# Optimization experiments

Measured on AMD Instinct MI355X. Metric: run time of the kernel, lower is better.

Reference implementation:

```python
import jax, jax.numpy as jnp
import numpy as np

N, E, DIN, HID, G, L = 50000, 200000, 128, 128, 64, 6
H1, H2 = 8, 4
EPS_LN, EPS_BN = 1e-5, 1e-5


def setup_inputs() -> dict:
    key = jax.random.key(0)
    ks = iter(jax.random.split(key, 32))
    def nrm(shape, scale=0.05):
        return jax.random.normal(next(ks), shape, dtype=jnp.float32) * scale
    z = lambda *s: jnp.zeros(s, jnp.float32)
    o = lambda *s: jnp.ones(s, jnp.float32)
    return {
        'x': jax.random.normal(next(ks), (N, DIN), dtype=jnp.float32),
        'edge_index': jax.random.randint(next(ks), (2, E), 0, N),
        'batch': jnp.sort(jax.random.randint(next(ks), (N,), 0, G)),
        'W1': nrm((DIN, H1 * HID)), 'a_src1': nrm((H1, HID)), 'a_dst1': nrm((H1, HID)), 'b1': z(H1 * HID),
        'W2': nrm((H1 * HID, H2 * HID)), 'a_src2': nrm((H2, HID)), 'a_dst2': nrm((H2, HID)), 'b2': z(H2 * HID),
        'W3': nrm((H2 * HID, HID)), 'b3': z(HID),
        'wq': nrm((L, HID, HID)), 'bq': z(L, HID), 'wk': nrm((L, HID, HID)), 'bk': z(L, HID),
        'wv': nrm((L, HID, HID)), 'bv': z(L, HID), 'wo': nrm((L, HID, HID)), 'bo': z(L, HID),
        'ln1g': o(L, HID), 'ln1b': z(L, HID), 'ln2g': o(L, HID), 'ln2b': z(L, HID),
        'wf1': nrm((L, HID, 4 * HID)), 'bf1': z(L, 4 * HID), 'wf2': nrm((L, 4 * HID, HID)), 'bf2': z(L, HID),
        'bn1_g': o(2 * HID), 'bn1_b': z(2 * HID),
        'fc1_w': nrm((2 * HID, HID // 2)), 'fc1_b': z(HID // 2),
        'bn2_g': o(HID // 2), 'bn2_b': z(HID // 2),
        'fc2_w': nrm((HID // 2, 2)), 'fc2_b': z(2),
    }


def _ln(x, g, b):
    mu = x.mean(-1, keepdims=True)
    v = ((x - mu) ** 2).mean(-1, keepdims=True)
    return (x - mu) * jax.lax.rsqrt(v + EPS_LN) * g + b


def _gat(x, src, dst, W, a_s, a_d, b, heads):
    # PyG GATConv: message src -> dst, segment softmax over incoming edges per dst.
    h = (x @ W).reshape(x.shape[0], heads, -1)           # [N, H, C]
    e = jax.nn.leaky_relu((h * a_s).sum(-1)[src] + (h * a_d).sum(-1)[dst], 0.2)  # [E, H]
    m = jax.ops.segment_max(e, dst, num_segments=N)
    ex = jnp.exp(e - jnp.where(jnp.isfinite(m), m, 0.0)[dst])
    s = jax.ops.segment_sum(ex, dst, num_segments=N)
    alpha = ex / (s[dst] + 1e-16)
    out = jax.ops.segment_sum(alpha[:, :, None] * h[src], dst, num_segments=N)
    return out.reshape(N, -1) + b


def _forward(x, edge_index, batch, W1, a_src1, a_dst1, b1, W2, a_src2, a_dst2, b2, W3, b3,
             wq, bq, wk, bk, wv, bv, wo, bo, ln1g, ln1b, ln2g, ln2b, wf1, bf1, wf2, bf2,
             bn1_g, bn1_b, fc1_w, fc1_b, bn2_g, bn2_b, fc2_w, fc2_b):
    loop = jnp.arange(N, dtype=edge_index.dtype)
    src = jnp.concatenate([edge_index[0], loop])          # add self-loops (PyG default)
    dst = jnp.concatenate([edge_index[1], loop])
    h = jax.nn.elu(_gat(x, src, dst, W1, a_src1, a_dst1, b1, H1))
    h = jax.nn.elu(_gat(h, src, dst, W2, a_src2, a_dst2, b2, H2))
    # GCNConv with symmetric normalization (self-loops already included)
    deg = jax.ops.segment_sum(jnp.ones(src.shape, h.dtype), dst, num_segments=N)
    dinv = jnp.where(deg > 0, jax.lax.rsqrt(jnp.maximum(deg, 1e-12)), 0.0)
    norm = dinv[src] * dinv[dst]
    h = jax.nn.elu(jax.ops.segment_sum(norm[:, None] * (h @ W3)[src], dst, num_segments=N) + b3)
    # TransformerEncoder over seq_len=1 (h3.unsqueeze(1)): softmax over one key == 1,
    # so MHA output == Wo @ (Wv h + bv) + bo exactly; q/k have no effect on the output.
    for l in range(L):
        sa = (h @ wv[l] + bv[l]) @ wo[l] + bo[l]
        h = _ln(h + sa, ln1g[l], ln1b[l])
        ff = jax.nn.gelu(h @ wf1[l] + bf1[l], approximate=False) @ wf2[l] + bf2[l]
        h = _ln(h + ff, ln2g[l], ln2b[l])
    # global mean / max pool over graphs
    cnt = jax.ops.segment_sum(jnp.ones((N,), h.dtype), batch, num_segments=G)
    hm = jax.ops.segment_sum(h, batch, num_segments=G) / jnp.maximum(cnt, 1.0)[:, None]
    hx = jax.ops.segment_max(h, batch, num_segments=G)
    hx = jnp.where(jnp.isfinite(hx), hx, 0.0)
    hc = jnp.concatenate([hm, hx], axis=1)                # [G, 2*HID]
    bn_s = 1.0 / np.sqrt(1.0 + EPS_BN)                    # eval BN: running stats (0, 1)
    hc = hc * bn_s * bn1_g + bn1_b
    hc = jax.nn.elu(hc @ fc1_w + fc1_b)
    hc = hc * bn_s * bn2_g + bn2_b
    return hc @ fc2_w + fc2_b                             # [G, 2]


def reference(x, edge_index, batch, W1, a_src1, a_dst1, b1, W2, a_src2, a_dst2, b2, W3, b3,
              wq, bq, wk, bk, wv, bv, wo, bo, ln1g, ln1b, ln2g, ln2b, wf1, bf1, wf2, bf2,
              bn1_g, bn1_b, fc1_w, fc1_b, bn2_g, bn2_b, fc2_w, fc2_b):
    return _forward(x, edge_index, batch, W1, a_src1, a_dst1, b1, W2, a_src2, a_dst2, b2, W3, b3,
                    wq, bq, wk, bk, wv, bv, wo, bo, ln1g, ln1b, ln2g, ln2b, wf1, bf1, wf2, bf2,
                    bn1_g, bn1_b, fc1_w, fc1_b, bn2_g, bn2_b, fc2_w, fc2_b)
```

## Files before the change

### kernel.cpp

```cpp
#include <hip/hip_runtime.h>
#include <hip/hip_bf16.h>
#include <math.h>

#define NN 50000
#define EE 200000
#define ET 250000
#define GG 64
#define LL 6

using short8 = __attribute__((ext_vector_type(8))) short;
using f32x4  = __attribute__((ext_vector_type(4))) float;
typedef unsigned short ushortT;

__device__ __forceinline__ float elu1(float x) { return x > 0.f ? x : expm1f(x); }
__device__ __forceinline__ float gelu_exact(float x) {
    return 0.5f * x * (1.f + erff(x * 0.70710678118654752440f));
}
__device__ __forceinline__ short f2bf(float f) {
    __hip_bfloat16 h = __float2bfloat16(f);
    return *reinterpret_cast<short*>(&h);
}
__device__ __forceinline__ float bf2f(ushortT u) {
    return __uint_as_float(((unsigned)u) << 16);
}

__global__ void count_deg_kernel(const int* __restrict__ ei, int* __restrict__ deg) {
    int e = blockIdx.x * 256 + threadIdx.x;
    if (e >= ET) return;
    int dst = (e < EE) ? ei[EE + e] : (e - EE);
    atomicAdd(&deg[dst], 1);
}

__global__ void scan_kernel(const int* __restrict__ deg, int* __restrict__ row_ptr, int n) {
    __shared__ int s[1024];
    int tid = threadIdx.x;
    const int per = (n + 1023) / 1024;
    int lo = tid * per, hi = min(lo + per, n);
    int sum = 0;
    for (int i = lo; i < hi; i++) sum += deg[i];
    s[tid] = sum;
    __syncthreads();
    for (int off = 1; off < 1024; off <<= 1) {
        int t = (tid >= off) ? s[tid - off] : 0;
        __syncthreads();
        s[tid] += t;
        __syncthreads();
    }
    int run = s[tid] - sum;
    for (int i = lo; i < hi; i++) { row_ptr[i] = run; run += deg[i]; }
    if (tid == 1023) row_ptr[n] = s[1023];
}

__global__ void fill_csr_kernel(const int* __restrict__ ei, const int* __restrict__ row_ptr,
                                int* __restrict__ cursor, int* __restrict__ edge_src) {
    int e = blockIdx.x * 256 + threadIdx.x;
    if (e >= ET) return;
    int src, dst;
    if (e < EE) { src = ei[e]; dst = ei[EE + e]; }
    else        { src = e - EE; dst = e - EE; }
    int pos = atomicAdd(&cursor[dst], 1);
    edge_src[row_ptr[dst] + pos] = src;
}

__global__ void dinv_kernel(const int* __restrict__ row_ptr, float* __restrict__ dinv) {
    int n = blockIdx.x * 256 + threadIdx.x;
    if (n >= NN) return;
    int d = row_ptr[n + 1] - row_ptr[n];
    dinv[n] = (d > 0) ? rsqrtf((float)d) : 0.f;
}

__global__ void wvwo_kernel(const float* __restrict__ wv, const float* __restrict__ wo,
                            const float* __restrict__ bv, const float* __restrict__ bo,
                            float* __restrict__ Wvo, float* __restrict__ bvo) {
    int l = blockIdx.y;
    const float* Wv = wv + l * 16384;
    const float* Wo = wo + l * 16384;
    int tid = blockIdx.x * 256 + threadIdx.x;
    if (tid < 16384) {
        int r = tid >> 7, c = tid & 127;
        float s = 0.f;
        for (int k = 0; k < 128; k++) s += Wv[r * 128 + k] * Wo[k * 128 + c];
        Wvo[l * 16384 + tid] = s;
    }
    if (blockIdx.x == 0 && threadIdx.x < 128) {
        int c = threadIdx.x;
        float s = bo[l * 128 + c];
        for (int k = 0; k < 128; k++) s += bv[l * 128 + k] * Wo[k * 128 + c];
        bvo[l * 128 + c] = s;
    }
}

__global__ void bprep_kernel(const float* __restrict__ B, short* __restrict__ Bp,
                             int K, int N, int ldb, long srcStride) {
    int layer = blockIdx.y;
    const float* Bsrc = B + srcStride * layer;
    short* Bd = Bp + (size_t)K * N * layer;
    int total = (K >> 5) * (N >> 4) * 64;
    int tid = blockIdx.x * 256 + threadIdx.x;
    if (tid >= total) return;
    int l = tid & 63;
    int rest = tid >> 6;
    int kbc = K >> 5;
    int kb = rest % kbc;
    int c16 = rest / kbc;
    int n = c16 * 16 + (l & 15);
    int kbase = kb * 32 + (l >> 4) * 8;
    short v[8];
#pragma unroll
    for (int j = 0; j < 8; j++) v[j] = f2bf(Bsrc[(size_t)(kbase + j) * ldb + n]);
    *(uint4*)(Bd + (size_t)tid * 8) = *(uint4*)v;
}

__global__ void cast_bf16_kernel(const float* __restrict__ in, short* __restrict__ out, int n4) {
    int i = blockIdx.x * 256 + threadIdx.x;
    if (i >= n4) return;
    float4 v = *(const float4*)(in + (size_t)i * 4);
    short s[4] = { f2bf(v.x), f2bf(v.y), f2bf(v.z), f2bf(v.w) };
    *(uint2*)(out + (size_t)i * 4) = *(uint2*)s;
}

template <int EPI, bool BIAS, bool OUTBF16, int NSPLIT, int KBC>
__global__ __launch_bounds__(256) void gemm_bf16_kernel(
    const short* __restrict__ A, const short* __restrict__ Bp,
    const float* __restrict__ bias, void* __restrict__ Cv,
    const float* __restrict__ a_s, const float* __restrict__ a_d,
    float* __restrict__ as_out, float* __restrict__ ad_out, int asH,
    const ushortT* __restrict__ Rres, const float* __restrict__ lng,
    const float* __restrict__ lnb, float* __restrict__ Qout,
    __hip_bfloat16* __restrict__ Qbout,
    int M, int K, int Nc) {
    __shared__ short Bs[(KBC > 0) ? KBC * 4096 : 8192];
    int t = threadIdx.x;
    int w = t >> 6, l = t & 63;
    int ln = l & 15, lq = l >> 4;
    int MBceil = (M + 63) >> 6;
    int bx = blockIdx.x;
    int xcd = bx & 7, idx = bx >> 3;
    int t2 = idx % NSPLIT;
    int mb = (idx / NSPLIT) * 8 + xcd;
    if (mb >= MBceil) return;
    int bm = mb * 64 + w * 16;
    int arow = bm + ln;
    bool aok = arow < M;
    int rowb = bm + lq * 4;
    const short* Ap = A + (size_t)arow * K + lq * 8;

    f32x4 acc[8];
#pragma unroll
    for (int j = 0; j < 8; j++) acc[j] = (f32x4){0.f, 0.f, 0.f, 0.f};

    if constexpr (KBC > 0) {
        {
            const uint4* src = (const uint4*)(Bp + (size_t)t2 * KBC * 4096);
            uint4* dst = (uint4*)Bs;
#pragma unroll
            for (int i = 0; i < KBC * 2; i++)
                dst[i * 256 + t] = src[i * 256 + t];
        }
        short8 af[KBC];
#pragma unroll
        for (int kb = 0; kb < KBC; kb++)
            af[kb] = aok ? *(const short8*)(Ap + kb * 32) : (short8){0,0,0,0,0,0,0,0};
        __syncthreads();
#pragma unroll
        for (int kb = 0; kb < KBC; kb++)
#pragma unroll
            for (int ct = 0; ct < 8; ct++) {
                short8 bfr = *(const short8*)(Bs + ((ct * KBC + kb) * 64 + l) * 8);
                acc[ct] = __builtin_amdgcn_mfma_f32_16x16x32_bf16(af[kb], bfr, acc[ct], 0, 0, 0);
            }
    } else {
        int kbc = K >> 5;
        int sct = t >> 5, spart = t & 31;
        auto stage = [&](int buf, int kb) {
            const uint4* src = (const uint4*)(Bp + ((size_t)(t2 * 8 + sct) * kbc + kb) * 512);
            uint4* dst = (uint4*)(Bs + buf * 4096 + sct * 512);
            dst[spart * 2]     = src[spart * 2];
            dst[spart * 2 + 1] = src[spart * 2 + 1];
        };
        stage(0, 0);
        __syncthreads();
        for (int kb = 0; kb < kbc; kb++) {
            if (kb + 1 < kbc) stage((kb + 1) & 1, kb + 1);
            short8 af = aok ? *(const short8*)(Ap + kb * 32) : (short8){0,0,0,0,0,0,0,0};
            const short* bsb = Bs + (kb & 1) * 4096;
#pragma unroll
            for (int ct = 0; ct < 8; ct++) {
                short8 bfr = *(const short8*)(bsb + (ct * 64 + l) * 8);
                acc[ct] = __builtin_amdgcn_mfma_f32_16x16x32_bf16(af, bfr, acc[ct], 0, 0, 0);
            }
            __syncthreads();
        }
    }

    if (EPI == 2) {
        const float* asv = a_s + t2 * 128;
        const float* adv = a_d + t2 * 128;
#pragma unroll
        for (int reg = 0; reg < 4; reg++) {
            float vs = 0.f, vd = 0.f;
#pragma unroll
            for (int ct = 0; ct < 8; ct++) {
                int colL = ct * 16 + ln;
                float av = acc[ct][reg];
                vs += av * asv[colL];
                vd += av * adv[colL];
            }
            vs += __shfl_xor(vs, 1); vs += __shfl_xor(vs, 2);
            vs += __shfl_xor(vs, 4); vs += __shfl_xor(vs, 8);
            vd += __shfl_xor(vd, 1); vd += __shfl_xor(vd, 2);
            vd += __shfl_xor(vd, 4); vd += __shfl_xor(vd, 8);
            int row = rowb + reg;
            if (ln == 0 && row < M) {
                as_out[(size_t)row * asH + t2] = vs;
                ad_out[(size_t)row * asH + t2] = vd;
            }
        }
    }
    if (EPI == 3) {
        float v[8][4];
#pragma unroll
        for (int ct = 0; ct < 8; ct++) {
            int col = ct * 16 + ln;
            float bv_ = bias[col];
#pragma unroll
            for (int reg = 0; reg < 4; reg++) {
                int row = rowb + reg;
                float r = (row < M) ? bf2f(Rres[(size_t)row * 128 + col]) : 0.f;
                v[ct][reg] = acc[ct][reg] + bv_ + r;
            }
        }
#pragma unroll
        for (int reg = 0; reg < 4; reg++) {
            float s = 0.f;
#pragma unroll
            for (int ct = 0; ct < 8; ct++) s += v[ct][reg];
            s += __shfl_xor(s, 1); s += __shfl_xor(s, 2);
            s += __shfl_xor(s, 4); s += __shfl_xor(s, 8);
            float mean = s * (1.f / 128.f);
            float s2 = 0.f;
#pragma unroll
            for (int ct = 0; ct < 8; ct++) { float d = v[ct][reg] - mean; s2 += d * d; }
            s2 += __shfl_xor(s2, 1); s2 += __shfl_xor(s2, 2);
            s2 += __shfl_xor(s2, 4); s2 += __shfl_xor(s2, 8);
            float rstd = rsqrtf(s2 * (1.f / 128.f) + 1e-5f);
            int row = rowb + reg;
            if (row < M) {
#pragma unroll
                for (int ct = 0; ct < 8; ct++) {
                    int col = ct * 16 + ln;
                    float o = (v[ct][reg] - mean) * rstd * lng[col] + lnb[col];
                    Qbout[(size_t)row * 128 + col] = __float2bfloat16(o);
                    if (Qout) Qout[(size_t)row * 128 + col] = o;
                }
            }
        }
    }
    if (EPI == 0 || EPI == 1 || EPI == 2) {
#pragma unroll
        for (int ct = 0; ct < 8; ct++) {
            int col = t2 * 128 + ct * 16 + ln;
            float bv_ = BIAS ? bias[col] : 0.f;
#pragma unroll
            for (int reg = 0; reg < 4; reg++) {
                int row = rowb + reg;
                if (row < M) {
                    float v = acc[ct][reg] + bv_;
                    if (EPI == 1) v = gelu_exact(v);
                    if (OUTBF16)
                        ((__hip_bfloat16*)Cv)[(size_t)row * Nc + col] = __float2bfloat16(v);
                    else
                        ((float*)Cv)[(size_t)row * Nc + col] = v;
                }
            }
        }
    }
}

template <int H>
__global__ __launch_bounds__(256) void gat_alpha_kernel(
    const float* __restrict__ as_, const float* __restrict__ ad_,
    const int* __restrict__ row_ptr, const int* __restrict__ edge_src,
    float* __restrict__ exA, float* __restrict__ exS, int n_nodes) {
    const int GS = 64 / H;
    int node = blockIdx.x * 4 + (threadIdx.x >> 6);
    if (node >= n_nodes) return;
    int l = threadIdx.x & 63;
    int h = l / GS;
    int lig = l % GS;
    int start = row_ptr[node];
    int deg = row_ptr[node + 1] - start;
    float adn = ad_[(size_t)node * H + h];
    float m = -1e30f;
    for (int j = lig; j < deg; j += GS) {
        int s = edge_src[start + j];
        float e = as_[(size_t)s * H + h] + adn;
        e = e > 0.f ? e : 0.2f * e;
        m = fmaxf(m, e);
    }
#pragma unroll
    for (int mask = 1; mask < GS; mask <<= 1)
        m = fmaxf(m, __shfl_xor(m, mask));
    float S = 0.f;
    for (int j = lig; j < deg; j += GS) {
        int s = edge_src[start + j];
        float e = as_[(size_t)s * H + h] + adn;
        e = e > 0.f ? e : 0.2f * e;
        float ex = expf(e - m);
        exA[(size_t)(start + j) * H + h] = ex;
        S += ex;
    }
#pragma unroll
    for (int mask = 1; mask < GS; mask <<= 1)
        S += __shfl_xor(S, mask);
    if (lig == 0) exS[(size_t)node * H + h] = S;
}

template <int H>
__global__ __launch_bounds__(256) void gat_agg2_kernel(
    const ushortT* __restrict__ hpre, const float* __restrict__ exA,
    const float* __restrict__ exS, const float* __restrict__ bias,
    const int* __restrict__ row_ptr, const int* __restrict__ edge_src,
    __hip_bfloat16* __restrict__ out, int n_nodes) {
    const int CPT = H;
    int node = blockIdx.x * 2 + (threadIdx.x >> 7);
    if (node >= n_nodes) return;
    int tt = threadIdx.x & 127;
    int c0 = tt * CPT;
    int hb = c0 >> 7;
    int start = row_ptr[node];
    int deg = row_ptr[node + 1] - start;
    float acc[CPT];
#pragma unroll
    for (int c = 0; c < CPT; c++) acc[c] = 0.f;
    for (int j = 0; j < deg; j++) {
        int s = edge_src[start + j];
        float a = exA[(size_t)(start + j) * H + hb];
        const ushortT* hp = hpre + (size_t)s * (H * 128) + c0;
        float hv[CPT];
        if (CPT == 8) {
            uint4 u = *(const uint4*)hp;
            hv[0] = bf2f((ushortT)(u.x & 0xffff)); hv[1] = bf2f((ushortT)(u.x >> 16));
            hv[2] = bf2f((ushortT)(u.y & 0xffff)); hv[3] = bf2f((ushortT)(u.y >> 16));
            hv[4] = bf2f((ushortT)(u.z & 0xffff)); hv[5] = bf2f((ushortT)(u.z >> 16));
            hv[6] = bf2f((ushortT)(u.w & 0xffff)); hv[7] = bf2f((ushortT)(u.w >> 16));
        } else {
            uint2 u = *(const uint2*)hp;
            hv[0] = bf2f((ushortT)(u.x & 0xffff)); hv[1] = bf2f((ushortT)(u.x >> 16));
            hv[2] = bf2f((ushortT)(u.y & 0xffff)); hv[3] = bf2f((ushortT)(u.y >> 16));
        }
#pragma unroll
        for (int c = 0; c < CPT; c++) acc[c] += a * hv[c];
    }
    float inv = 1.f / (exS[(size_t)node * H + hb] + 1e-16f);
#pragma unroll
    for (int c = 0; c < CPT; c++)
        out[(size_t)node * (H * 128) + c0 + c] =
            __float2bfloat16(elu1(acc[c] * inv + bias[c0 + c]));
}

__global__ __launch_bounds__(256) void gcn_agg_kernel(
    const ushortT* __restrict__ hp, const float* __restrict__ dinv,
    const float* __restrict__ b3, const int* __restrict__ row_ptr,
    const int* __restrict__ edge_src,
    __hip_bfloat16* __restrict__ outb, int n_nodes) {
    int node = blockIdx.x * 2 + (threadIdx.x >> 7);
    int c = threadIdx.x & 127;
    if (node >= n_nodes) return;
    int start = row_ptr[node];
    int deg = row_ptr[node + 1] - start;
    float dn = dinv[node];
    float acc = 0.f;
    for (int j = 0; j < deg; j++) {
        int s = edge_src[start + j];
        acc += dinv[s] * dn * bf2f(hp[(size_t)s * 128 + c]);
    }
    outb[(size_t)node * 128 + c] = __float2bfloat16(elu1(acc + b3[c]));
}

__global__ void pool1_kernel(const float* __restrict__ Q, const int* __restrict__ batch,
                             float* __restrict__ psum, float* __restrict__ pmax, int n_nodes) {
    int g = blockIdx.x, seg = blockIdx.y;
    int c = threadIdx.x;
    int lo, hi;
    {
        int l = 0, h = n_nodes;
        while (l < h) { int mid = (l + h) >> 1; if (batch[mid] < g) l = mid + 1; else h = mid; }
        lo = l;
        l = lo; h = n_nodes;
        while (l < h) { int mid = (l + h) >> 1; if (batch[mid] < g + 1) l = mid + 1; else h = mid; }
        hi = l;
    }
    int len = hi - lo;
    int a = lo + (int)((long)len * seg / 8);
    int b = lo + (int)((long)len * (seg + 1) / 8);
    float s = 0.f, mx = -INFINITY;
    for (int n = a; n < b; n++) {
        float v = Q[(size_t)n * 128 + c];
        s += v;
        mx = fmaxf(mx, v);
    }
    psum[(g * 8 + seg) * 128 + c] = s;
    pmax[(g * 8 + seg) * 128 + c] = mx;
}

__global__ void pool2_kernel(const float* __restrict__ psum, const float* __restrict__ pmax,
                             const int* __restrict__ batch,
                             const float* __restrict__ bn1g, const float* __restrict__ bn1b,
                             float* __restrict__ hc, int n_nodes) {
    int g = blockIdx.x;
    int c = threadIdx.x;
    int lo, hi;
    {
        int l = 0, h = n_nodes;
        while (l < h) { int mid = (l + h) >> 1; if (batch[mid] < g) l = mid + 1; else h = mid; }
        lo = l;
        l = lo; h = n_nodes;
        while (l < h) { int mid = (l + h) >> 1; if (batch[mid] < g + 1) l = mid + 1; else h = mid; }
        hi = l;
    }
    int cnt = hi - lo;
    float s = 0.f, mx = -INFINITY;
    for (int seg = 0; seg < 8; seg++) {
        s += psum[(g * 8 + seg) * 128 + c];
        mx = fmaxf(mx, pmax[(g * 8 + seg) * 128 + c]);
    }
    float hm = s / fmaxf((float)cnt, 1.f);
    float hx = (cnt > 0 && isfinite(mx)) ? mx : 0.f;
    const float bn_s = 0.99999500003749968f;
    hc[g * 256 + c]       = hm * bn_s * bn1g[c] + bn1b[c];
    hc[g * 256 + 128 + c] = hx * bn_s * bn1g[128 + c] + bn1b[128 + c];
}

__global__ void head_kernel(const float* __restrict__ hc,
                            const float* __restrict__ fc1w, const float* __restrict__ fc1b,
                            const float* __restrict__ bn2g, const float* __restrict__ bn2b,
                            const float* __restrict__ fc2w, const float* __restrict__ fc2b,
                            float* __restrict__ out) {
    int g = blockIdx.x;
    int j = threadIdx.x;
    const float bn_s = 0.99999500003749968f;
    float acc = fc1b[j];
    for (int i = 0; i < 256; i++) acc += hc[g * 256 + i] * fc1w[i * 64 + j];
    acc = elu1(acc);
    acc = acc * bn_s * bn2g[j] + bn2b[j];
    __shared__ float sv[64];
    sv[j] = acc;
    __syncthreads();
    if (j < 2) {
        float o = fc2b[j];
        for (int i = 0; i < 64; i++) o += sv[i] * fc2w[i * 2 + j];
        out[g * 2 + j] = o;
    }
}

extern "C" void kernel_launch(void* const* d_in, const int* in_sizes, int n_in,
                              void* d_out, int out_size, void* d_ws, size_t ws_size,
                              hipStream_t stream) {
    const float* x    = (const float*)d_in[0];
    const int*   ei   = (const int*)d_in[1];
    const int*   batch= (const int*)d_in[2];
    const float* W1   = (const float*)d_in[3];
    const float* as1  = (const float*)d_in[4];
    const float* ad1  = (const float*)d_in[5];
    const float* b1   = (const float*)d_in[6];
    const float* W2   = (const float*)d_in[7];
    const float* as2  = (const float*)d_in[8];
    const float* ad2  = (const float*)d_in[9];
    const float* b2   = (const float*)d_in[10];
    const float* W3   = (const float*)d_in[11];
    const float* b3   = (const float*)d_in[12];
    const float* wv   = (const float*)d_in[17];
    const float* bv   = (const float*)d_in[18];
    const float* wo   = (const float*)d_in[19];
    const float* bo   = (const float*)d_in[20];
    const float* ln1g = (const float*)d_in[21];
    const float* ln1b = (const float*)d_in[22];
    const float* ln2g = (const float*)d_in[23];
    const float* ln2b = (const float*)d_in[24];
    const float* wf1  = (const float*)d_in[25];
    const float* bf1  = (const float*)d_in[26];
    const float* wf2  = (const float*)d_in[27];
    const float* bf2  = (const float*)d_in[28];
    const float* bn1g = (const float*)d_in[29];
    const float* bn1b = (const float*)d_in[30];
    const float* fc1w = (const float*)d_in[31];
    const float* fc1b = (const float*)d_in[32];
    const float* bn2g = (const float*)d_in[33];
    const float* bn2b = (const float*)d_in[34];
    const float* fc2w = (const float*)d_in[35];
    const float* fc2b = (const float*)d_in[36];
    float* out = (float*)d_out;

    char* wsb = (char*)d_ws;
    short* xb    = (short*)wsb;
    float* exAf  = (float*)wsb;
    float* exSf  = (float*)(wsb + 8000000);
    short* h1pre = (short*)(wsb + 12800000);
    short* h2pre = (short*)(wsb + 12800000);
    short* h3pre = (short*)(wsb + 12800000);
    short* FFb   = (short*)(wsb + 25600000);
    short* bh1   = (short*)(wsb + 115200000);
    short* bh2   = (short*)(wsb + 115200000);
    float* fQ    = (float*)(wsb + 128000000);
    short* Qb    = (short*)(wsb + 153600000);
    char* tail = wsb + 217600000;
    short* W1p  = (short*)tail;  tail += 262144;
    short* W2p  = (short*)tail;  tail += 1048576;
    short* W3p  = (short*)tail;  tail += 131072;
    short* Wvop = (short*)tail;  tail += 196608;
    short* wf1p = (short*)tail;  tail += 786432;
    short* wf2p = (short*)tail;  tail += 786432;
    float* Wvo  = (float*)tail;  tail += 393216;
    float* bvo  = (float*)tail;  tail += 3072;
    float* fAS  = (float*)tail;  tail += 1600000;
    float* fAD  = (float*)tail;  tail += 1600000;
    float* fDv  = (float*)tail;  tail += 200000;
    float* psum = (float*)tail;  tail += 262144;
    float* pmax = (float*)tail;  tail += 262144;
    float* fHC  = (float*)tail;  tail += 65536;
    int* iDeg   = (int*)tail;    tail += 200000;
    int* iRP    = (int*)tail;    tail += 200004;
    int* iCur   = (int*)tail;    tail += 200000;
    int* iES    = (int*)tail;    tail += 1000000;

    hipMemsetAsync(iDeg, 0, NN * sizeof(int), stream);
    hipMemsetAsync(iCur, 0, NN * sizeof(int), stream);

    count_deg_kernel<<<(ET + 255) / 256, 256, 0, stream>>>(ei, iDeg);
    scan_kernel<<<1, 1024, 0, stream>>>(iDeg, iRP, NN);
    fill_csr_kernel<<<(ET + 255) / 256, 256, 0, stream>>>(ei, iRP, iCur, iES);
    dinv_kernel<<<(NN + 255) / 256, 256, 0, stream>>>(iRP, fDv);

    wvwo_kernel<<<dim3(64, 6), 256, 0, stream>>>(wv, wo, bv, bo, Wvo, bvo);
    auto bprep = [&](const float* B, short* Bp, int K, int N, int ldb, long sStride, int layers) {
        int total = (K >> 5) * (N >> 4) * 64;
        dim3 grid((total + 255) / 256, layers);
        bprep_kernel<<<grid, 256, 0, stream>>>(B, Bp, K, N, ldb, sStride);
    };
    bprep(W1, W1p, 128, 1024, 1024, 0, 1);
    bprep(W2, W2p, 1024, 512, 512, 0, 1);
    bprep(W3, W3p, 512, 128, 128, 0, 1);
    bprep(Wvo, Wvop, 128, 128, 128, 16384, 6);
    bprep(wf1, wf1p, 128, 512, 512, 65536, 6);
    bprep(wf2, wf2p, 512, 128, 128, 65536, 6);
    cast_bf16_kernel<<<(NN * 128 / 4 + 255) / 256, 256, 0, stream>>>(x, xb, NN * 128 / 4);

    const int MB64 = (NN + 63) / 64;
    const int MBp = ((MB64 + 7) / 8) * 8;

    gemm_bf16_kernel<2, false, true, 8, 4><<<MBp * 8, 256, 0, stream>>>(
        xb, W1p, nullptr, h1pre, as1, ad1, fAS, fAD, 8,
        nullptr, nullptr, nullptr, nullptr, nullptr, NN, 128, 1024);
    gat_alpha_kernel<8><<<(NN + 3) / 4, 256, 0, stream>>>(
        fAS, fAD, iRP, iES, exAf, exSf, NN);
    gat_agg2_kernel<8><<<(NN + 1) / 2, 256, 0, stream>>>(
        (const ushortT*)h1pre, exAf, exSf, b1, iRP, iES, (__hip_bfloat16*)bh1, NN);
    gemm_bf16_kernel<2, false, true, 4, 0><<<MBp * 4, 256, 0, stream>>>(
        bh1, W2p, nullptr, h2pre, as2, ad2, fAS, fAD, 4,
        nullptr, nullptr, nullptr, nullptr, nullptr, NN, 1024, 512);
    gat_alpha_kernel<4><<<(NN + 3) / 4, 256, 0, stream>>>(
        fAS, fAD, iRP, iES, exAf, exSf, NN);
    gat_agg2_kernel<4><<<(NN + 1) / 2, 256, 0, stream>>>(
        (const ushortT*)h2pre, exAf, exSf, b2, iRP, iES, (__hip_bfloat16*)bh2, NN);
    gemm_bf16_kernel<0, false, true, 1, 0><<<MBp, 256, 0, stream>>>(
        bh2, W3p, nullptr, h3pre, nullptr, nullptr, nullptr, nullptr, 0,
        nullptr, nullptr, nullptr, nullptr, nullptr, NN, 512, 128);
    gcn_agg_kernel<<<(NN + 1) / 2, 256, 0, stream>>>(
        (const ushortT*)h3pre, fDv, b3, iRP, iES, (__hip_bfloat16*)Qb, NN);
    for (int l = 0; l < LL; l++) {
        gemm_bf16_kernel<3, true, false, 1, 4><<<MBp, 256, 0, stream>>>(
            Qb, Wvop + l * 16384, bvo + l * 128, nullptr, nullptr, nullptr, nullptr, nullptr, 0,
            (const ushortT*)Qb, ln1g + l * 128, ln1b + l * 128, nullptr, (__hip_bfloat16*)Qb,
            NN, 128, 128);
        gemm_bf16_kernel<1, true, true, 4, 4><<<MBp * 4, 256, 0, stream>>>(
            Qb, wf1p + l * 65536, bf1 + l * 512, FFb, nullptr, nullptr, nullptr, nullptr, 0,
            nullptr, nullptr, nullptr, nullptr, nullptr, NN, 128, 512);
        gemm_bf16_kernel<3, true, false, 1, 0><<<MBp, 256, 0, stream>>>(
            FFb, wf2p + l * 65536, bf2 + l * 128, nullptr, nullptr, nullptr, nullptr, nullptr, 0,
            (const ushortT*)Qb, ln2g + l * 128, ln2b + l * 128,
            (l == LL - 1) ? fQ : nullptr, (__hip_bfloat16*)Qb, NN, 512, 128);
    }
    pool1_kernel<<<dim3(GG, 8), 128, 0, stream>>>(fQ, batch, psum, pmax, NN);
    pool2_kernel<<<GG, 128, 0, stream>>>(psum, pmax, batch, bn1g, bn1b, fHC, NN);
    head_kernel<<<GG, 64, 0, stream>>>(fHC, fc1w, fc1b, bn2g, bn2b, fc2w, fc2b, out);
}
```

Measured before the change: 1.364 ms.

## Tile GAT features into 32-column node-major slabs for cache-local aggregation

The GAT projection GEMMs now write their bf16 outputs in a tiled layout of 32-column slabs, each stored node-major. A new tiled aggregation kernel walks one slab at a time, with XCD-aware block ordering, so the random neighbour gathers stay inside a smaller working set that fits in cache. Attention coefficients are stored head-major. The next GEMMs read the tiled activations directly through a new A-tile load path. The GCN aggregation is also software-pipelined, prefetching 8 neighbours ahead with a launch-bounds occupancy hint, which adds register pressure and extra kernel template variants.

Result: faster. 1.308 ms (-4.1%).

```diff
diff --git a/kernel.cpp b/kernel.cpp
--- a/kernel.cpp
+++ b/kernel.cpp
@@ -22,6 +22,16 @@
 }
 __device__ __forceinline__ float bf2f(ushortT u) {
     return __uint_as_float(((unsigned)u) << 16);
+}
+__device__ __forceinline__ void accum8(float* acc, float a, uint4 d) {
+    acc[0] += a * bf2f((ushortT)(d.x & 0xffff));
+    acc[1] += a * bf2f((ushortT)(d.x >> 16));
+    acc[2] += a * bf2f((ushortT)(d.y & 0xffff));
+    acc[3] += a * bf2f((ushortT)(d.y >> 16));
+    acc[4] += a * bf2f((ushortT)(d.z & 0xffff));
+    acc[5] += a * bf2f((ushortT)(d.z >> 16));
+    acc[6] += a * bf2f((ushortT)(d.w & 0xffff));
+    acc[7] += a * bf2f((ushortT)(d.w >> 16));
 }
 
 __global__ void count_deg_kernel(const int* __restrict__ ei, int* __restrict__ deg) {
@@ -119,7 +129,8 @@
     *(uint2*)(out + (size_t)i * 4) = *(uint2*)s;
 }
 
-template <int EPI, bool BIAS, bool OUTBF16, int NSPLIT, int KBC>
+template <int EPI, bool BIAS, bool OUTBF16, int NSPLIT, int KBC,
+          bool TMAJ = false, bool ATILE32 = false>
 __global__ __launch_bounds__(256) void gemm_bf16_kernel(
     const short* __restrict__ A, const short* __restrict__ Bp,
     const float* __restrict__ bias, void* __restrict__ Cv,
@@ -145,6 +156,16 @@
     int rowb = bm + lq * 4;
     const short* Ap = A + (size_t)arow * K + lq * 8;
 
+    auto aload = [&](int kb) -> short8 {
+        if (!aok) return (short8){0, 0, 0, 0, 0, 0, 0, 0};
+        const short* p;
+        if constexpr (ATILE32)
+            p = A + ((size_t)kb * M + arow) * 32 + lq * 8;
+        else
+            p = Ap + kb * 32;
+        return *(const short8*)p;
+    };
+
     f32x4 acc[8];
 #pragma unroll
     for (int j = 0; j < 8; j++) acc[j] = (f32x4){0.f, 0.f, 0.f, 0.f};
@@ -160,7 +181,7 @@
         short8 af[KBC];
 #pragma unroll
         for (int kb = 0; kb < KBC; kb++)
-            af[kb] = aok ? *(const short8*)(Ap + kb * 32) : (short8){0,0,0,0,0,0,0,0};
+            af[kb] = aload(kb);
         __syncthreads();
 #pragma unroll
         for (int kb = 0; kb < KBC; kb++)
@@ -182,7 +203,7 @@
         __syncthreads();
         for (int kb = 0; kb < kbc; kb++) {
             if (kb + 1 < kbc) stage((kb + 1) & 1, kb + 1);
-            short8 af = aok ? *(const short8*)(Ap + kb * 32) : (short8){0,0,0,0,0,0,0,0};
+            short8 af = aload(kb);
             const short* bsb = Bs + (kb & 1) * 4096;
 #pragma unroll
             for (int ct = 0; ct < 8; ct++) {
@@ -267,10 +288,16 @@
                 if (row < M) {
                     float v = acc[ct][reg] + bv_;
                     if (EPI == 1) v = gelu_exact(v);
-                    if (OUTBF16)
-                        ((__hip_bfloat16*)Cv)[(size_t)row * Nc + col] = __float2bfloat16(v);
-                    else
+                    if (OUTBF16) {
+                        size_t addr;
+                        if constexpr (TMAJ)
+                            addr = ((size_t)(col >> 5) * M + row) * 32 + (col & 31);
+                        else
+                            addr = (size_t)row * Nc + col;
+                        ((__hip_bfloat16*)Cv)[addr] = __float2bfloat16(v);
+                    } else {
                         ((float*)Cv)[(size_t)row * Nc + col] = v;
+                    }
                 }
             }
         }
@@ -307,59 +334,51 @@
         float e = as_[(size_t)s * H + h] + adn;
         e = e > 0.f ? e : 0.2f * e;
         float ex = expf(e - m);
-        exA[(size_t)(start + j) * H + h] = ex;
+        exA[(size_t)h * ET + (start + j)] = ex;
         S += ex;
     }
 #pragma unroll
     for (int mask = 1; mask < GS; mask <<= 1)
         S += __shfl_xor(S, mask);
-    if (lig == 0) exS[(size_t)node * H + h] = S;
-}
-
-template <int H>
-__global__ __launch_bounds__(256) void gat_agg2_kernel(
-    const ushortT* __restrict__ hpre, const float* __restrict__ exA,
+    if (lig == 0) exS[(size_t)h * n_nodes + node] = S;
+}
+
+__global__ __launch_bounds__(256) void gat_agg_tiled_kernel(
+    const ushortT* __restrict__ hT, const float* __restrict__ exA,
     const float* __restrict__ exS, const float* __restrict__ bias,
     const int* __restrict__ row_ptr, const int* __restrict__ edge_src,
-    __hip_bfloat16* __restrict__ out, int n_nodes) {
-    const int CPT = H;
-    int node = blockIdx.x * 2 + (threadIdx.x >> 7);
+    __hip_bfloat16* __restrict__ outT, int n_nodes, int NB) {
+    int bx = blockIdx.x;
+    int xcd = bx & 7, rest = bx >> 3;
+    int tl = rest / NB, nb = rest - tl * NB;
+    int tile = tl * 8 + xcd;
+    int nl = threadIdx.x >> 2, q = threadIdx.x & 3;
+    int node = nb * 64 + nl;
     if (node >= n_nodes) return;
-    int tt = threadIdx.x & 127;
-    int c0 = tt * CPT;
-    int hb = c0 >> 7;
+    int hb = tile >> 2;
+    const ushortT* __restrict__ base = hT + (size_t)tile * n_nodes * 32 + q * 8;
+    const float* __restrict__ exAh = exA + (size_t)hb * ET;
     int start = row_ptr[node];
     int deg = row_ptr[node + 1] - start;
-    float acc[CPT];
-#pragma unroll
-    for (int c = 0; c < CPT; c++) acc[c] = 0.f;
+    float acc[8];
+#pragma unroll
+    for (int c = 0; c < 8; c++) acc[c] = 0.f;
     for (int j = 0; j < deg; j++) {
         int s = edge_src[start + j];
-        float a = exA[(size_t)(start + j) * H + hb];
-        const ushortT* hp = hpre + (size_t)s * (H * 128) + c0;
-        float hv[CPT];
-        if (CPT == 8) {
-            uint4 u = *(const uint4*)hp;
-            hv[0] = bf2f((ushortT)(u.x & 0xffff)); hv[1] = bf2f((ushortT)(u.x >> 16));
-            hv[2] = bf2f((ushortT)(u.y & 0xffff)); hv[3] = bf2f((ushortT)(u.y >> 16));
-            hv[4] = bf2f((ushortT)(u.z & 0xffff)); hv[5] = bf2f((ushortT)(u.z >> 16));
-            hv[6] = bf2f((ushortT)(u.w & 0xffff)); hv[7] = bf2f((ushortT)(u.w >> 16));
-        } else {
-            uint2 u = *(const uint2*)hp;
-            hv[0] = bf2f((ushortT)(u.x & 0xffff)); hv[1] = bf2f((ushortT)(u.x >> 16));
-            hv[2] = bf2f((ushortT)(u.y & 0xffff)); hv[3] = bf2f((ushortT)(u.y >> 16));
-        }
-#pragma unroll
-        for (int c = 0; c < CPT; c++) acc[c] += a * hv[c];
-    }
-    float inv = 1.f / (exS[(size_t)node * H + hb] + 1e-16f);
-#pragma unroll
-    for (int c = 0; c < CPT; c++)
-        out[(size_t)node * (H * 128) + c0 + c] =
-            __float2bfloat16(elu1(acc[c] * inv + bias[c0 + c]));
-}
-
-__global__ __launch_bounds__(256) void gcn_agg_kernel(
+        float a = exAh[start + j];
+        uint4 d = *(const uint4*)(base + (size_t)s * 32);
+        accum8(acc, a, d);
+    }
+    float inv = 1.f / (exS[(size_t)hb * n_nodes + node] + 1e-16f);
+    const float* bp = bias + tile * 32 + q * 8;
+    short o[8];
+#pragma unroll
+    for (int c = 0; c < 8; c++)
+        o[c] = f2bf(elu1(acc[c] * inv + bp[c]));
+    *(uint4*)(outT + ((size_t)tile * n_nodes + node) * 32 + q * 8) = *(uint4*)o;
+}
+
+__global__ __launch_bounds__(256, 2) void gcn_agg_kernel(
     const ushortT* __restrict__ hp, const float* __restrict__ dinv,
     const float* __restrict__ b3, const int* __restrict__ row_ptr,
     const int* __restrict__ edge_src,
@@ -371,9 +390,40 @@
     int deg = row_ptr[node + 1] - start;
     float dn = dinv[node];
     float acc = 0.f;
-    for (int j = 0; j < deg; j++) {
-        int s = edge_src[start + j];
-        acc += dinv[s] * dn * bf2f(hp[(size_t)s * 128 + c]);
+    auto LS = [&](int j) { return edge_src[start + min(j, deg - 1)]; };
+    int s0 = LS(0), s1 = LS(1), s2 = LS(2), s3 = LS(3);
+    int s4 = LS(4), s5 = LS(5), s6 = LS(6), s7 = LS(7);
+    auto HW = [&](int s, int j, float& h, float& w) {
+        h = bf2f(hp[(size_t)s * 128 + c]);
+        w = (j < deg) ? dinv[s] * dn : 0.f;
+    };
+    float h0, h1, h2, h3, h4, h5, h6, h7;
+    float w0, w1, w2, w3, w4, w5, w6, w7;
+    HW(s0, 0, h0, w0); HW(s1, 1, h1, w1); HW(s2, 2, h2, w2); HW(s3, 3, h3, w3);
+    HW(s4, 4, h4, w4); HW(s5, 5, h5, w5); HW(s6, 6, h6, w6); HW(s7, 7, h7, w7);
+    int j0 = 0;
+    while (true) {
+        int jn = j0 + 8;
+        bool more = jn < deg;
+        float g0, g1, g2, g3, g4, g5, g6, g7;
+        float v0 = 0.f, v1 = 0.f, v2 = 0.f, v3 = 0.f;
+        float v4 = 0.f, v5 = 0.f, v6 = 0.f, v7 = 0.f;
+        if (more) {
+            int t0 = LS(jn),     t1 = LS(jn + 1), t2 = LS(jn + 2), t3 = LS(jn + 3);
+            int t4 = LS(jn + 4), t5 = LS(jn + 5), t6 = LS(jn + 6), t7 = LS(jn + 7);
+            HW(t0, jn,     g0, v0); HW(t1, jn + 1, g1, v1);
+            HW(t2, jn + 2, g2, v2); HW(t3, jn + 3, g3, v3);
+            HW(t4, jn + 4, g4, v4); HW(t5, jn + 5, g5, v5);
+            HW(t6, jn + 6, g6, v6); HW(t7, jn + 7, g7, v7);
+        }
+        acc += w0 * h0 + w1 * h1 + w2 * h2 + w3 * h3
+             + w4 * h4 + w5 * h5 + w6 * h6 + w7 * h7;
+        if (!more) break;
+        h0 = g0; h1 = g1; h2 = g2; h3 = g3;
+        h4 = g4; h5 = g5; h6 = g6; h7 = g7;
+        w0 = v0; w1 = v1; w2 = v2; w3 = v3;
+        w4 = v4; w5 = v5; w6 = v6; w7 = v7;
+        j0 = jn;
     }
     outb[(size_t)node * 128 + c] = __float2bfloat16(elu1(acc + b3[c]));
 }
@@ -496,8 +546,8 @@
     short* xb    = (short*)wsb;
     float* exAf  = (float*)wsb;
     float* exSf  = (float*)(wsb + 8000000);
-    short* h1pre = (short*)(wsb + 12800000);
-    short* h2pre = (short*)(wsb + 12800000);
+    short* h1t   = (short*)(wsb + 12800000);
+    short* h2t   = (short*)(wsb + 12800000);
     short* h3pre = (short*)(wsb + 12800000);
     short* FFb   = (short*)(wsb + 25600000);
     short* bh1   = (short*)(wsb + 115200000);
@@ -548,22 +598,23 @@
 
     const int MB64 = (NN + 63) / 64;
     const int MBp = ((MB64 + 7) / 8) * 8;
-
-    gemm_bf16_kernel<2, false, true, 8, 4><<<MBp * 8, 256, 0, stream>>>(
-        xb, W1p, nullptr, h1pre, as1, ad1, fAS, fAD, 8,
+    const int NB = (NN + 63) / 64;
+
+    gemm_bf16_kernel<2, false, true, 8, 4, true, false><<<MBp * 8, 256, 0, stream>>>(
+        xb, W1p, nullptr, h1t, as1, ad1, fAS, fAD, 8,
         nullptr, nullptr, nullptr, nullptr, nullptr, NN, 128, 1024);
     gat_alpha_kernel<8><<<(NN + 3) / 4, 256, 0, stream>>>(
         fAS, fAD, iRP, iES, exAf, exSf, NN);
-    gat_agg2_kernel<8><<<(NN + 1) / 2, 256, 0, stream>>>(
-        (const ushortT*)h1pre, exAf, exSf, b1, iRP, iES, (__hip_bfloat16*)bh1, NN);
-    gemm_bf16_kernel<2, false, true, 4, 0><<<MBp * 4, 256, 0, stream>>>(
-        bh1, W2p, nullptr, h2pre, as2, ad2, fAS, fAD, 4,
+    gat_agg_tiled_kernel<<<4 * NB * 8, 256, 0, stream>>>(
+        (const ushortT*)h1t, exAf, exSf, b1, iRP, iES, (__hip_bfloat16*)bh1, NN, NB);
+    gemm_bf16_kernel<2, false, true, 4, 0, true, true><<<MBp * 4, 256, 0, stream>>>(
+        bh1, W2p, nullptr, h2t, as2, ad2, fAS, fAD, 4,
         nullptr, nullptr, nullptr, nullptr, nullptr, NN, 1024, 512);
     gat_alpha_kernel<4><<<(NN + 3) / 4, 256, 0, stream>>>(
         fAS, fAD, iRP, iES, exAf, exSf, NN);
-    gat_agg2_kernel<4><<<(NN + 1) / 2, 256, 0, stream>>>(
-        (const ushortT*)h2pre, exAf, exSf, b2, iRP, iES, (__hip_bfloat16*)bh2, NN);
-    gemm_bf16_kernel<0, false, true, 1, 0><<<MBp, 256, 0, stream>>>(
+    gat_agg_tiled_kernel<<<2 * NB * 8, 256, 0, stream>>>(
+        (const ushortT*)h2t, exAf, exSf, b2, iRP, iES, (__hip_bfloat16*)bh2, NN, NB);
+    gemm_bf16_kernel<0, false, true, 1, 0, false, true><<<MBp, 256, 0, stream>>>(
         bh2, W3p, nullptr, h3pre, nullptr, nullptr, nullptr, nullptr, 0,
         nullptr, nullptr, nullptr, nullptr, nullptr, NN, 512, 128);
     gcn_agg_kernel<<<(NN + 1) / 2, 256, 0, stream>>>(
```
